# Kernel tuning notes

Hardware: AMD Instinct MI355X
Metric: run time of the kernel (lower is better)

The kernel has to match this reference:

```python
import jax, jax.numpy as jnp
import numpy as np

L = 8        # num_layers
D = 1024     # hidden_dim
H = 16       # num_heads
DH = D // H  # head dim
W = 8        # window_size (= cyclic group order for 'C4')
DIN = 512    # input_dim
ACT = 256    # action_dim
B, S = 8, 2048
EPS = 1e-5


def setup_inputs() -> dict:
    key = jax.random.key(0)
    ks = jax.random.split(key, 16)
    std = 0.02
    def n(k, shape):
        return jax.random.normal(k, shape, jnp.float32) * std
    return {
        "observation": jax.random.normal(ks[0], (B, S, DIN), jnp.float32),
        "We": n(ks[1], (DIN, D)), "be": jnp.zeros((D,), jnp.float32),
        "Wq": n(ks[2], (L, D, D)), "bq": jnp.zeros((L, D), jnp.float32),
        "Wk": n(ks[3], (L, D, D)), "bk": jnp.zeros((L, D), jnp.float32),
        "Wv": n(ks[4], (L, D, D)), "bv": jnp.zeros((L, D), jnp.float32),
        "Wo": n(ks[5], (L, D, D)), "bo": jnp.zeros((L, D), jnp.float32),
        "ln1g": jnp.ones((L, D), jnp.float32), "ln1b": jnp.zeros((L, D), jnp.float32),
        "ln2g": jnp.ones((L, D), jnp.float32), "ln2b": jnp.zeros((L, D), jnp.float32),
        "W1": n(ks[6], (L, D, 4 * D)), "b1": jnp.zeros((L, 4 * D), jnp.float32),
        "W2": n(ks[7], (L, 4 * D, D)), "b2": jnp.zeros((L, D), jnp.float32),
        "Wout": n(ks[8], (D, ACT)), "bout": jnp.zeros((ACT,), jnp.float32),
    }


def _layernorm(x, g, b):
    mu = x.mean(-1, keepdims=True)
    var = ((x - mu) ** 2).mean(-1, keepdims=True)
    return (x - mu) * jax.lax.rsqrt(var + EPS) * g + b


def _psead_attn(h, Wq, bq, Wk, bk, Wv, bv, Wo, bo):
    # h: [B, S, D]; window the sequence, attend within each window with
    # attention logits symmetrized over the cyclic group C_W acting on
    # window positions: S_sym[i,j] = mean_g S[g(i), g(j)].
    b, s, _ = h.shape
    nw = s // W
    def heads(x):  # [B,S,D] -> [B,nW,H,W,DH]
        return x.reshape(b, nw, W, H, DH).transpose(0, 1, 3, 2, 4)
    q = heads(h @ Wq + bq)
    k = heads(h @ Wk + bk)
    v = heads(h @ Wv + bv)
    scores = jnp.einsum("bnhid,bnhjd->bnhij", q, k) / np.sqrt(DH).astype(np.float32)
    # cyclic symmetrization (group order W = 8, small fixed loop)
    sym = jnp.mean(
        jnp.stack([jnp.roll(scores, (-g, -g), axis=(-2, -1)) for g in range(W)]),
        axis=0)
    attn = jax.nn.softmax(sym, axis=-1)
    out = jnp.einsum("bnhij,bnhjd->bnhid", attn, v)
    out = out.transpose(0, 1, 3, 2, 4).reshape(b, s, D)
    return out @ Wo + bo


def reference(observation, We, be, Wq, bq, Wk, bk, Wv, bv, Wo, bo,
              ln1g, ln1b, ln2g, ln2b, W1, b1, W2, b2, Wout, bout):
    x = observation @ We + be  # [B, S, D]
    for l in range(L):
        h = _layernorm(x, ln1g[l], ln1b[l])
        x = x + _psead_attn(h, Wq[l], bq[l], Wk[l], bk[l], Wv[l], bv[l], Wo[l], bo[l])
        h2 = _layernorm(x, ln2g[l], ln2b[l])
        x = x + (jax.nn.relu(h2 @ W1[l] + b1[l]) @ W2[l] + b2[l])
    return x.mean(axis=1) @ Wout + bout  # [B, action_dim]
```

## Files before the change

### kernel.cpp

```cpp
#include <hip/hip_runtime.h>
#include <stdint.h>

typedef __bf16 bf16x8 __attribute__((ext_vector_type(8)));
typedef float  f32x4  __attribute__((ext_vector_type(4)));

#define DEV static __device__ __forceinline__

DEV float b2f(unsigned short u) {
    unsigned int v = ((unsigned int)u) << 16;
    return __builtin_bit_cast(float, v);
}
DEV unsigned short f2b(float f) {
    unsigned int u = __builtin_bit_cast(unsigned int, f);
    u += 0x7fffu + ((u >> 16) & 1u);
    return (unsigned short)(u >> 16);
}
DEV void gload_lds16(const void* g, void* l) {
    __builtin_amdgcn_global_load_lds(
        (__attribute__((address_space(1))) void*)(void*)g,
        (__attribute__((address_space(3))) void*)l, 16, 0, 0);
}

__global__ void cvt_f32_bf16(const float* __restrict__ in,
                             unsigned short* __restrict__ out, int n4) {
    int i = blockIdx.x * 256 + threadIdx.x;
    if (i < n4) {
        float4 v = ((const float4*)in)[i];
        ushort4 o;
        o.x = f2b(v.x); o.y = f2b(v.y); o.z = f2b(v.z); o.w = f2b(v.w);
        ((ushort4*)out)[i] = o;
    }
}

__global__ void transpose_cvt(const float* __restrict__ in,
                              unsigned short* __restrict__ out, int K, int N) {
    __shared__ float tile[32][33];
    int nb = blockIdx.x, kb = blockIdx.y;
    int tx = threadIdx.x, ty = threadIdx.y;
#pragma unroll
    for (int i = 0; i < 4; ++i) {
        int k = kb * 32 + ty + i * 8;
        int n = nb * 32 + tx;
        tile[ty + i * 8][tx] = in[(size_t)k * N + n];
    }
    __syncthreads();
#pragma unroll
    for (int i = 0; i < 4; ++i) {
        int n = nb * 32 + ty + i * 8;
        int k = kb * 32 + tx;
        out[(size_t)n * K + k] = f2b(tile[tx][ty + i * 8]);
    }
}

template <int EPI>
__global__ __launch_bounds__(256, 2)
void gemm_bt(const unsigned short* __restrict__ A,
             const unsigned short* __restrict__ BT,
             const float* __restrict__ bias,
             void* __restrict__ Cout, int M, int N, int K) {
    __shared__ alignas(16) unsigned short As[128 * 32];
    __shared__ alignas(16) unsigned short Bs[128 * 32];

    const int tid = threadIdx.x;
    const int lane = tid & 63;
    const int w = tid >> 6;
    const int wr = w >> 1, wc = w & 1;
    const int bm = blockIdx.x, bn = blockIdx.y;

    f32x4 acc[4][4];
#pragma unroll
    for (int i = 0; i < 4; ++i)
#pragma unroll
        for (int j = 0; j < 4; ++j)
#pragma unroll
            for (int r = 0; r < 4; ++r) acc[i][j][r] = 0.f;

    const int off0 = (w)*1024 + lane * 16;
    const int off1 = (w + 4) * 1024 + lane * 16;
    const int r0 = off0 >> 6, c0 = off0 & 63;
    const int r1 = off1 >> 6, c1 = off1 & 63;

    const char* Ab0 = (const char*)A + ((size_t)(bm * 128 + r0) * K) * 2 + c0;
    const char* Ab1 = (const char*)A + ((size_t)(bm * 128 + r1) * K) * 2 + c1;
    const char* Bb0 = (const char*)BT + ((size_t)(bn * 128 + r0) * K) * 2 + c0;
    const char* Bb1 = (const char*)BT + ((size_t)(bn * 128 + r1) * K) * 2 + c1;

    char* lA0 = (char*)As + (w)*1024;
    char* lA1 = (char*)As + (w + 4) * 1024;
    char* lB0 = (char*)Bs + (w)*1024;
    char* lB1 = (char*)Bs + (w + 4) * 1024;

    const int rr = lane & 15;
    const int ko = (lane >> 4) * 8;
    const unsigned short* Ard = As + (wr * 64 + rr) * 32 + ko;
    const unsigned short* Brd = Bs + (wc * 64 + rr) * 32 + ko;

    const int nk = K >> 5;
    for (int kt = 0; kt < nk; ++kt) {
        const size_t kb2 = (size_t)kt * 64;
        __syncthreads();
        gload_lds16(Ab0 + kb2, lA0);
        gload_lds16(Ab1 + kb2, lA1);
        gload_lds16(Bb0 + kb2, lB0);
        gload_lds16(Bb1 + kb2, lB1);
        __syncthreads();

        bf16x8 af[4], bg[4];
#pragma unroll
        for (int i = 0; i < 4; ++i) {
            af[i] = *(const bf16x8*)(const void*)(Ard + i * 16 * 32);
            bg[i] = *(const bf16x8*)(const void*)(Brd + i * 16 * 32);
        }
#pragma unroll
        for (int i = 0; i < 4; ++i)
#pragma unroll
            for (int j = 0; j < 4; ++j)
                acc[i][j] = __builtin_amdgcn_mfma_f32_16x16x32_bf16(
                    af[i], bg[j], acc[i][j], 0, 0, 0);
    }

    const int g4 = lane >> 4;
#pragma unroll
    for (int i = 0; i < 4; ++i) {
#pragma unroll
        for (int j = 0; j < 4; ++j) {
            const int col = bn * 128 + wc * 64 + j * 16 + rr;
            const float bv = bias[col];
#pragma unroll
            for (int r = 0; r < 4; ++r) {
                const int row = bm * 128 + wr * 64 + i * 16 + g4 * 4 + r;
                float v = acc[i][j][r] + bv;
                size_t idx = (size_t)row * N + col;
                if (EPI == 0) {
                    ((float*)Cout)[idx] = v;
                } else if (EPI == 1) {
                    ((unsigned short*)Cout)[idx] = f2b(v);
                } else if (EPI == 2) {
                    ((unsigned short*)Cout)[idx] = f2b(v > 0.f ? v : 0.f);
                } else {
                    ((float*)Cout)[idx] += v;
                }
            }
        }
    }
}

__global__ __launch_bounds__(256)
void ln_kernel(const float* __restrict__ x, const float* __restrict__ g,
               const float* __restrict__ b, unsigned short* __restrict__ out) {
    const int row = blockIdx.x;
    const float* xr = x + (size_t)row * 1024;
    float4 v = ((const float4*)xr)[threadIdx.x];
    float s = v.x + v.y + v.z + v.w;
    float s2 = v.x * v.x + v.y * v.y + v.z * v.z + v.w * v.w;
#pragma unroll
    for (int m = 1; m < 64; m <<= 1) {
        s += __shfl_xor(s, m);
        s2 += __shfl_xor(s2, m);
    }
    __shared__ float red[8];
    int wv = threadIdx.x >> 6, lane = threadIdx.x & 63;
    if (lane == 0) { red[wv] = s; red[4 + wv] = s2; }
    __syncthreads();
    s = red[0] + red[1] + red[2] + red[3];
    s2 = red[4] + red[5] + red[6] + red[7];
    float mu = s * (1.f / 1024.f);
    float var = s2 * (1.f / 1024.f) - mu * mu;
    float rs = rsqrtf(var + 1e-5f);
    float4 gv = ((const float4*)g)[threadIdx.x];
    float4 bv = ((const float4*)b)[threadIdx.x];
    ushort4 o;
    o.x = f2b((v.x - mu) * rs * gv.x + bv.x);
    o.y = f2b((v.y - mu) * rs * gv.y + bv.y);
    o.z = f2b((v.z - mu) * rs * gv.z + bv.z);
    o.w = f2b((v.w - mu) * rs * gv.w + bv.w);
    ((ushort4*)(out + (size_t)row * 1024))[threadIdx.x] = o;
}

__global__ __launch_bounds__(256)
void attn_kernel(const unsigned short* __restrict__ q,
                 const unsigned short* __restrict__ k,
                 const unsigned short* __restrict__ v,
                 unsigned short* __restrict__ ao) {
    const int gid = blockIdx.x * 4 + (threadIdx.x >> 6);
    const int lane = threadIdx.x & 63;
    const int b = gid >> 12;
    const int rem = gid & 4095;
    const int win = rem >> 4;
    const int head = rem & 15;
    const size_t base = ((size_t)(b * 2048 + win * 8)) * 1024 + head * 64 + lane;

    float qf[8], kf[8], vf[8];
#pragma unroll
    for (int i = 0; i < 8; ++i) {
        qf[i] = b2f(q[base + i * 1024]);
        kf[i] = b2f(k[base + i * 1024]);
        vf[i] = b2f(v[base + i * 1024]);
    }
    float c[8];
#pragma unroll
    for (int d = 0; d < 8; ++d) {
        float s = 0.f;
#pragma unroll
        for (int i = 0; i < 8; ++i) s += qf[i] * kf[(i + d) & 7];
        c[d] = s;
    }
#pragma unroll
    for (int m = 1; m < 64; m <<= 1)
#pragma unroll
        for (int d = 0; d < 8; ++d) c[d] += __shfl_xor(c[d], m);
    float mx = -1e30f;
#pragma unroll
    for (int d = 0; d < 8; ++d) { c[d] *= (1.f / 64.f); mx = fmaxf(mx, c[d]); }
    float den = 0.f;
#pragma unroll
    for (int d = 0; d < 8; ++d) { c[d] = expf(c[d] - mx); den += c[d]; }
    float rden = 1.f / den;
#pragma unroll
    for (int i = 0; i < 8; ++i) {
        float o = 0.f;
#pragma unroll
        for (int d = 0; d < 8; ++d) o += c[d] * vf[(i + d) & 7];
        ao[base + i * 1024] = f2b(o * rden);
    }
}

__global__ void zero_kernel(float* p, int n) {
    int i = blockIdx.x * 256 + threadIdx.x;
    if (i < n) p[i] = 0.f;
}
__global__ void mean_partial(const float* __restrict__ x, float* __restrict__ xsum) {
    int b = blockIdx.x, dc = blockIdx.y, sc = blockIdx.z;
    int d = dc * 256 + threadIdx.x;
    float s = 0.f;
    for (int i = 0; i < 256; ++i)
        s += x[((size_t)(b * 2048 + sc * 256 + i)) * 1024 + d];
    atomicAdd(&xsum[b * 1024 + d], s);
}
__global__ void final_gemm(const float* __restrict__ xsum,
                           const float* __restrict__ Wout,
                           const float* __restrict__ bout,
                           float* __restrict__ out) {
    int b = blockIdx.x, a = threadIdx.x;
    float s = 0.f;
    for (int d = 0; d < 1024; ++d) s += xsum[b * 1024 + d] * Wout[d * 256 + a];
    out[b * 256 + a] = s * (1.f / 2048.f) + bout[a];
}

extern "C" void kernel_launch(void* const* d_in, const int* in_sizes, int n_in,
                              void* d_out, int out_size, void* d_ws, size_t ws_size,
                              hipStream_t stream) {
    const float* obs  = (const float*)d_in[0];
    const float* We   = (const float*)d_in[1];
    const float* be   = (const float*)d_in[2];
    const float* Wq   = (const float*)d_in[3];
    const float* bq   = (const float*)d_in[4];
    const float* Wk   = (const float*)d_in[5];
    const float* bk   = (const float*)d_in[6];
    const float* Wv   = (const float*)d_in[7];
    const float* bv   = (const float*)d_in[8];
    const float* Wo   = (const float*)d_in[9];
    const float* bo   = (const float*)d_in[10];
    const float* ln1g = (const float*)d_in[11];
    const float* ln1b = (const float*)d_in[12];
    const float* ln2g = (const float*)d_in[13];
    const float* ln2b = (const float*)d_in[14];
    const float* W1   = (const float*)d_in[15];
    const float* b1   = (const float*)d_in[16];
    const float* W2   = (const float*)d_in[17];
    const float* b2   = (const float*)d_in[18];
    const float* Wout = (const float*)d_in[19];
    const float* bout = (const float*)d_in[20];
    float* out = (float*)d_out;

    char* p = (char*)d_ws;
    float* x = (float*)p;                 p += (size_t)16384 * 1024 * 4;
    unsigned short* h = (unsigned short*)p; p += (size_t)16384 * 1024 * 2;
    unsigned short* qb = (unsigned short*)p;
    unsigned short* kb = qb + (size_t)16384 * 1024;
    unsigned short* vb = qb + (size_t)2 * 16384 * 1024;
    unsigned short* aob = qb + (size_t)3 * 16384 * 1024;
    unsigned short* mb = qb;              p += (size_t)16384 * 4096 * 2;
    unsigned short* obsb = (unsigned short*)p; p += (size_t)16384 * 512 * 2;
    unsigned short* WeT = (unsigned short*)p;  p += (size_t)512 * 1024 * 2;
    unsigned short* WqT = (unsigned short*)p;  p += (size_t)1024 * 1024 * 2;
    unsigned short* WkT = (unsigned short*)p;  p += (size_t)1024 * 1024 * 2;
    unsigned short* WvT = (unsigned short*)p;  p += (size_t)1024 * 1024 * 2;
    unsigned short* WoT = (unsigned short*)p;  p += (size_t)1024 * 1024 * 2;
    unsigned short* W1T = (unsigned short*)p;  p += (size_t)1024 * 4096 * 2;
    unsigned short* W2T = (unsigned short*)p;  p += (size_t)4096 * 1024 * 2;
    float* xsum = (float*)p;              p += 8 * 1024 * 4;

    dim3 tb(32, 8);

    cvt_f32_bf16<<<8192, 256, 0, stream>>>(obs, obsb, 2097152);
    transpose_cvt<<<dim3(1024 / 32, 512 / 32), tb, 0, stream>>>(We, WeT, 512, 1024);
    gemm_bt<0><<<dim3(128, 8), 256, 0, stream>>>(obsb, WeT, be, x, 16384, 1024, 512);

    for (int l = 0; l < 8; ++l) {
        const size_t dd = (size_t)l * 1024 * 1024;
        transpose_cvt<<<dim3(32, 32), tb, 0, stream>>>(Wq + dd, WqT, 1024, 1024);
        transpose_cvt<<<dim3(32, 32), tb, 0, stream>>>(Wk + dd, WkT, 1024, 1024);
        transpose_cvt<<<dim3(32, 32), tb, 0, stream>>>(Wv + dd, WvT, 1024, 1024);
        transpose_cvt<<<dim3(32, 32), tb, 0, stream>>>(Wo + dd, WoT, 1024, 1024);
        transpose_cvt<<<dim3(128, 32), tb, 0, stream>>>(W1 + (size_t)l * 1024 * 4096, W1T, 1024, 4096);
        transpose_cvt<<<dim3(32, 128), tb, 0, stream>>>(W2 + (size_t)l * 4096 * 1024, W2T, 4096, 1024);

        ln_kernel<<<16384, 256, 0, stream>>>(x, ln1g + l * 1024, ln1b + l * 1024, h);
        gemm_bt<1><<<dim3(128, 8), 256, 0, stream>>>(h, WqT, bq + l * 1024, qb, 16384, 1024, 1024);
        gemm_bt<1><<<dim3(128, 8), 256, 0, stream>>>(h, WkT, bk + l * 1024, kb, 16384, 1024, 1024);
        gemm_bt<1><<<dim3(128, 8), 256, 0, stream>>>(h, WvT, bv + l * 1024, vb, 16384, 1024, 1024);
        attn_kernel<<<8192, 256, 0, stream>>>(qb, kb, vb, aob);
        gemm_bt<3><<<dim3(128, 8), 256, 0, stream>>>(aob, WoT, bo + l * 1024, x, 16384, 1024, 1024);
        ln_kernel<<<16384, 256, 0, stream>>>(x, ln2g + l * 1024, ln2b + l * 1024, h);
        gemm_bt<2><<<dim3(128, 32), 256, 0, stream>>>(h, W1T, b1 + l * 4096, mb, 16384, 4096, 1024);
        gemm_bt<3><<<dim3(128, 8), 256, 0, stream>>>(mb, W2T, b2 + l * 1024, x, 16384, 1024, 4096);
    }

    zero_kernel<<<32, 256, 0, stream>>>(xsum, 8192);
    mean_partial<<<dim3(8, 4, 8), 256, 0, stream>>>(x, xsum);
    final_gemm<<<8, 256, 0, stream>>>(xsum, Wout, bout, out);
}
```

Measured before the change: 5.085 ms.

## Replace GEMM with 256x256 double-buffered, swizzled, ping-pong scheduled MFMA kernel

Replaces the 128x128, single-buffered GEMM with a 512-thread kernel that computes 256x256 tiles over a 64-wide K step. LDS is double-buffered with an XOR swizzle, reads use inline ds_read_b128, and global-to-LDS staging is interleaved with quarter-tile MFMA groups using barriers, waitcnt and setprio. A block-index remap is added for L2 locality. The aim is to raise operand reuse and overlap loads with compute in every projection and FFN GEMM. In exchange it adds heavy register pressure and brittle hand scheduling that assumes dimensions divisible by 256 and an even number of K tiles.

```diff
diff --git a/kernel.cpp b/kernel.cpp
--- a/kernel.cpp
+++ b/kernel.cpp
@@ -3,6 +3,7 @@
 
 typedef __bf16 bf16x8 __attribute__((ext_vector_type(8)));
 typedef float  f32x4  __attribute__((ext_vector_type(4)));
+typedef int    i32x4  __attribute__((ext_vector_type(4)));
 
 #define DEV static __device__ __forceinline__
 
@@ -19,6 +20,9 @@
     __builtin_amdgcn_global_load_lds(
         (__attribute__((address_space(1))) void*)(void*)g,
         (__attribute__((address_space(3))) void*)l, 16, 0, 0);
+}
+DEV unsigned lds_addr(const void* p) {
+    return (unsigned)(size_t)(__attribute__((address_space(3))) const void*)p;
 }
 
 __global__ void cvt_f32_bf16(const float* __restrict__ in,
@@ -52,85 +56,145 @@
     }
 }
 
+#define DSR(dst, a) asm volatile("ds_read_b128 %0, %1" : "=v"(dst) : "v"(a))
+#define BB(x) __builtin_bit_cast(bf16x8, x)
+#define BAR __builtin_amdgcn_s_barrier()
+#define LGKM0 { asm volatile("s_waitcnt lgkmcnt(0)" ::: "memory"); \
+                __builtin_amdgcn_sched_barrier(0); }
+#define VMC4 asm volatile("s_waitcnt vmcnt(4)" ::: "memory")
+#define SP1 __builtin_amdgcn_s_setprio(1)
+#define SP0 { __builtin_amdgcn_sched_barrier(0); __builtin_amdgcn_s_setprio(0); }
+
+#define READ_A(c, mh) { const unsigned _ba = rowA + (c)*32768u + (mh)*8192u; \
+  _Pragma("unroll") for (int i = 0; i < 4; ++i) { \
+    DSR(aS[i][0], _ba + i*2048u + off0); \
+    DSR(aS[i][1], _ba + i*2048u + off1); } }
+#define READ_B(c, nh) { const unsigned _bb = rowB + (c)*32768u + (nh)*4096u; \
+  _Pragma("unroll") for (int j = 0; j < 2; ++j) { \
+    DSR(bS[nh][j][0], _bb + j*2048u + off0); \
+    DSR(bS[nh][j][1], _bb + j*2048u + off1); } }
+#define STAGE_A(buf, half, kt) { \
+  const char* _s = srcA + (size_t)(half)*128*K2 + (size_t)(kt)*128; \
+  char* _d = ldsA + (buf)*32768 + (half)*16384 + w*1024; \
+  gload_lds16(_s, _d); gload_lds16(_s + 64*K2, _d + 8192); }
+#define STAGE_B(buf, half, kt) { \
+  const char* _s = srcB + (size_t)(half)*128*K2 + (size_t)(kt)*128; \
+  char* _d = ldsB + (buf)*32768 + (half)*16384 + w*1024; \
+  gload_lds16(_s, _d); gload_lds16(_s + 64*K2, _d + 8192); }
+#define MMAQ(mh, nh) \
+  _Pragma("unroll") for (int i = 0; i < 4; ++i) \
+  _Pragma("unroll") for (int j = 0; j < 2; ++j) { \
+    acc[(mh)*4+i][(nh)*2+j] = __builtin_amdgcn_mfma_f32_16x16x32_bf16( \
+        BB(aS[i][0]), BB(bS[nh][j][0]), acc[(mh)*4+i][(nh)*2+j], 0, 0, 0); \
+    acc[(mh)*4+i][(nh)*2+j] = __builtin_amdgcn_mfma_f32_16x16x32_bf16( \
+        BB(aS[i][1]), BB(bS[nh][j][1]), acc[(mh)*4+i][(nh)*2+j], 0, 0, 0); }
+
 template <int EPI>
-__global__ __launch_bounds__(256, 2)
-void gemm_bt(const unsigned short* __restrict__ A,
+__global__ __launch_bounds__(512, 2)
+void gemm256(const unsigned short* __restrict__ A,
              const unsigned short* __restrict__ BT,
              const float* __restrict__ bias,
-             void* __restrict__ Cout, int M, int N, int K) {
-    __shared__ alignas(16) unsigned short As[128 * 32];
-    __shared__ alignas(16) unsigned short Bs[128 * 32];
+             void* __restrict__ Cout, int N, int K, int nbnShift) {
+    __shared__ alignas(16) unsigned short As[2 * 256 * 64];
+    __shared__ alignas(16) unsigned short Bs[2 * 256 * 64];
 
     const int tid = threadIdx.x;
     const int lane = tid & 63;
     const int w = tid >> 6;
-    const int wr = w >> 1, wc = w & 1;
-    const int bm = blockIdx.x, bn = blockIdx.y;
-
-    f32x4 acc[4][4];
-#pragma unroll
-    for (int i = 0; i < 4; ++i)
+    const int wr = w >> 2, wc = w & 3;
+
+    const int nwg = gridDim.x;
+    const int q = nwg >> 3;
+    const int sw = ((int)blockIdx.x & 7) * q + ((int)blockIdx.x >> 3);
+    const int bm = sw >> nbnShift;
+    const int bn = sw & ((1 << nbnShift) - 1);
+
+    const size_t K2 = (size_t)K * 2;
+
+    const int lr = lane >> 3;
+    const unsigned scol = (unsigned)(((lane & 7) * 16) ^ ((lr & 7) << 4));
+    const char* srcA = (const char*)A + (size_t)(bm * 256 + w * 8 + lr) * K2 + scol;
+    const char* srcB = (const char*)BT + (size_t)(bn * 256 + w * 8 + lr) * K2 + scol;
+    char* ldsA = (char*)As;
+    char* ldsB = (char*)Bs;
+
+    const unsigned asA = lds_addr(As);
+    const unsigned bsB = lds_addr(Bs);
+    const int rr = lane & 15, kq = lane >> 4;
+    const unsigned xr = (unsigned)((rr & 7) << 4);
+    const unsigned off0 = ((unsigned)(kq * 16)) ^ xr;
+    const unsigned off1 = ((unsigned)(64 + kq * 16)) ^ xr;
+    const unsigned rowA = asA + (unsigned)((wr * 128 + rr) * 128);
+    const unsigned rowB = bsB + (unsigned)((wc * 64 + rr) * 128);
+
+    f32x4 acc[8][4];
+#pragma unroll
+    for (int i = 0; i < 8; ++i)
 #pragma unroll
         for (int j = 0; j < 4; ++j)
 #pragma unroll
             for (int r = 0; r < 4; ++r) acc[i][j][r] = 0.f;
 
-    const int off0 = (w)*1024 + lane * 16;
-    const int off1 = (w + 4) * 1024 + lane * 16;
-    const int r0 = off0 >> 6, c0 = off0 & 63;
-    const int r1 = off1 >> 6, c1 = off1 & 63;
-
-    const char* Ab0 = (const char*)A + ((size_t)(bm * 128 + r0) * K) * 2 + c0;
-    const char* Ab1 = (const char*)A + ((size_t)(bm * 128 + r1) * K) * 2 + c1;
-    const char* Bb0 = (const char*)BT + ((size_t)(bn * 128 + r0) * K) * 2 + c0;
-    const char* Bb1 = (const char*)BT + ((size_t)(bn * 128 + r1) * K) * 2 + c1;
-
-    char* lA0 = (char*)As + (w)*1024;
-    char* lA1 = (char*)As + (w + 4) * 1024;
-    char* lB0 = (char*)Bs + (w)*1024;
-    char* lB1 = (char*)Bs + (w + 4) * 1024;
-
-    const int rr = lane & 15;
-    const int ko = (lane >> 4) * 8;
-    const unsigned short* Ard = As + (wr * 64 + rr) * 32 + ko;
-    const unsigned short* Brd = Bs + (wc * 64 + rr) * 32 + ko;
-
-    const int nk = K >> 5;
-    for (int kt = 0; kt < nk; ++kt) {
-        const size_t kb2 = (size_t)kt * 64;
-        __syncthreads();
-        gload_lds16(Ab0 + kb2, lA0);
-        gload_lds16(Ab1 + kb2, lA1);
-        gload_lds16(Bb0 + kb2, lB0);
-        gload_lds16(Bb1 + kb2, lB1);
-        __syncthreads();
-
-        bf16x8 af[4], bg[4];
-#pragma unroll
-        for (int i = 0; i < 4; ++i) {
-            af[i] = *(const bf16x8*)(const void*)(Ard + i * 16 * 32);
-            bg[i] = *(const bf16x8*)(const void*)(Brd + i * 16 * 32);
-        }
-#pragma unroll
-        for (int i = 0; i < 4; ++i)
-#pragma unroll
-            for (int j = 0; j < 4; ++j)
-                acc[i][j] = __builtin_amdgcn_mfma_f32_16x16x32_bf16(
-                    af[i], bg[j], acc[i][j], 0, 0, 0);
-    }
-
-    const int g4 = lane >> 4;
-#pragma unroll
-    for (int i = 0; i < 4; ++i) {
+    i32x4 aS[4][2], bS[2][2][2];
+
+    const int nt = K >> 6;
+    const int nu = nt >> 1;
+
+    STAGE_A(0, 0, 0); STAGE_A(0, 1, 0);
+    STAGE_B(0, 0, 0); STAGE_B(0, 1, 0);
+    STAGE_B(1, 0, 1); STAGE_B(1, 1, 1);
+    VMC4;
+    BAR;
+
+    for (int u = 0; u < nu; ++u) {
+        const int T = 2 * u;
+        const int t1 = T + 1;
+        const int t2 = (T + 2 < nt) ? T + 2 : nt - 1;
+        const int t3 = (T + 3 < nt) ? T + 3 : nt - 1;
+
+        READ_A(0, 0); READ_B(0, 0);
+        STAGE_A(1, 0, t1);
+        BAR; LGKM0;
+        SP1; MMAQ(0, 0); SP0; BAR;
+        READ_B(0, 1);
+        STAGE_A(1, 1, t1);
+        BAR; LGKM0;
+        SP1; MMAQ(0, 1); SP0; BAR;
+        READ_A(0, 1);
+        STAGE_B(0, 0, t2);
+        BAR; LGKM0;
+        SP1; MMAQ(1, 1); SP0; BAR;
+        STAGE_B(0, 1, t2);
+        VMC4; BAR;
+        SP1; MMAQ(1, 0); SP0; BAR;
+        READ_A(1, 0); READ_B(1, 0);
+        STAGE_A(0, 0, t2);
+        BAR; LGKM0;
+        SP1; MMAQ(0, 0); SP0; BAR;
+        READ_B(1, 1);
+        STAGE_A(0, 1, t2);
+        BAR; LGKM0;
+        SP1; MMAQ(0, 1); SP0; BAR;
+        READ_A(1, 1);
+        STAGE_B(1, 0, t3);
+        BAR; LGKM0;
+        SP1; MMAQ(1, 1); SP0; BAR;
+        STAGE_B(1, 1, t3);
+        VMC4; BAR;
+        SP1; MMAQ(1, 0); SP0; BAR;
+    }
+
+#pragma unroll
+    for (int i = 0; i < 8; ++i) {
+        const int row = bm * 256 + wr * 128 + i * 16 + kq * 4;
 #pragma unroll
         for (int j = 0; j < 4; ++j) {
-            const int col = bn * 128 + wc * 64 + j * 16 + rr;
+            const int col = bn * 256 + wc * 64 + j * 16 + rr;
             const float bv = bias[col];
 #pragma unroll
             for (int r = 0; r < 4; ++r) {
-                const int row = bm * 128 + wr * 64 + i * 16 + g4 * 4 + r;
                 float v = acc[i][j][r] + bv;
-                size_t idx = (size_t)row * N + col;
+                size_t idx = (size_t)(row + r) * N + col;
                 if (EPI == 0) {
                     ((float*)Cout)[idx] = v;
                 } else if (EPI == 1) {
@@ -295,7 +359,7 @@
 
     cvt_f32_bf16<<<8192, 256, 0, stream>>>(obs, obsb, 2097152);
     transpose_cvt<<<dim3(1024 / 32, 512 / 32), tb, 0, stream>>>(We, WeT, 512, 1024);
-    gemm_bt<0><<<dim3(128, 8), 256, 0, stream>>>(obsb, WeT, be, x, 16384, 1024, 512);
+    gemm256<0><<<256, 512, 0, stream>>>(obsb, WeT, be, x, 1024, 512, 2);
 
     for (int l = 0; l < 8; ++l) {
         const size_t dd = (size_t)l * 1024 * 1024;
@@ -307,14 +371,14 @@
         transpose_cvt<<<dim3(32, 128), tb, 0, stream>>>(W2 + (size_t)l * 4096 * 1024, W2T, 4096, 1024);
 
         ln_kernel<<<16384, 256, 0, stream>>>(x, ln1g + l * 1024, ln1b + l * 1024, h);
-        gemm_bt<1><<<dim3(128, 8), 256, 0, stream>>>(h, WqT, bq + l * 1024, qb, 16384, 1024, 1024);
-        gemm_bt<1><<<dim3(128, 8), 256, 0, stream>>>(h, WkT, bk + l * 1024, kb, 16384, 1024, 1024);
-        gemm_bt<1><<<dim3(128, 8), 256, 0, stream>>>(h, WvT, bv + l * 1024, vb, 16384, 1024, 1024);
+        gemm256<1><<<256, 512, 0, stream>>>(h, WqT, bq + l * 1024, qb, 1024, 1024, 2);
+        gemm256<1><<<256, 512, 0, stream>>>(h, WkT, bk + l * 1024, kb, 1024, 1024, 2);
+        gemm256<1><<<256, 512, 0, stream>>>(h, WvT, bv + l * 1024, vb, 1024, 1024, 2);
         attn_kernel<<<8192, 256, 0, stream>>>(qb, kb, vb, aob);
-        gemm_bt<3><<<dim3(128, 8), 256, 0, stream>>>(aob, WoT, bo + l * 1024, x, 16384, 1024, 1024);
+        gemm256<3><<<256, 512, 0, stream>>>(aob, WoT, bo + l * 1024, x, 1024, 1024, 2);
         ln_kernel<<<16384, 256, 0, stream>>>(x, ln2g + l * 1024, ln2b + l * 1024, h);
-        gemm_bt<2><<<dim3(128, 32), 256, 0, stream>>>(h, W1T, b1 + l * 4096, mb, 16384, 4096, 1024);
-        gemm_bt<3><<<dim3(128, 8), 256, 0, stream>>>(mb, W2T, b2 + l * 1024, x, 16384, 1024, 4096);
+        gemm256<2><<<1024, 512, 0, stream>>>(h, W1T, b1 + l * 4096, mb, 4096, 1024, 4);
+        gemm256<3><<<256, 512, 0, stream>>>(mb, W2T, b2 + l * 1024, x, 1024, 4096, 2);
     }
 
     zero_kernel<<<32, 256, 0, stream>>>(xsum, 8192);
```

Result: slower. 5.276 ms (+3.8%).
